# Kernel tuning notes

Measured on AMD Instinct MI355X. Metric: run time of the kernel, lower is better.

## Reference

```python
import jax, jax.numpy as jnp
import numpy as np
import math

B, N, D, H = 4, 512, 256, 8
DH = D // H


def setup_inputs() -> dict:
    key = jax.random.key(0)
    ks = jax.random.split(key, 10)
    s = 1.0 / math.sqrt(D)
    return {
        "h": jax.random.normal(ks[0], (B, N, D), jnp.float32),
        "p": jax.random.uniform(ks[1], (B, N, 2), jnp.float32) * 100.0,
        "side_id": jax.random.randint(ks[2], (B, N), 0, 2),
        "mask": jnp.ones((B, N), dtype=bool),
        # weights stored in 'apply' orientation: y = x @ W (+ b)
        "Wq": jax.random.normal(ks[3], (D, D), jnp.float32) * s,
        "Wk": jax.random.normal(ks[4], (D, D), jnp.float32) * s,
        "Wv": jax.random.normal(ks[5], (D, D), jnp.float32) * s,
        "Wo": jax.random.normal(ks[6], (D, D), jnp.float32) * s,
        "W1": jax.random.normal(ks[7], (4, D), jnp.float32) * 0.5,
        "b1": jnp.zeros((D,), jnp.float32),
        "W2": jax.random.normal(ks[8], (D, H), jnp.float32) * s,
        "b2": jnp.zeros((H,), jnp.float32),
    }


def reference(h, p, side_id, mask, Wq, Wk, Wv, Wo, W1, b1, W2, b2):
    # zero out masked players
    h = jnp.where(mask[..., None], h, 0.0)  # [B,N,D]

    q = (h @ Wq).reshape(B, N, H, DH)
    k = (h @ Wk).reshape(B, N, H, DH)
    v = (h @ Wv).reshape(B, N, H, DH)

    # pairwise relative-position features [B,N,N,4]
    dp = p[:, :, None, :] - p[:, None, :, :]               # [B,N,N,2]
    dist = jnp.clip(jnp.linalg.norm(dp, axis=-1, keepdims=True), 1e-6)
    is_team = (side_id[:, :, None] == side_id[:, None, :]).astype(h.dtype)[..., None]
    feat = jnp.concatenate([dp, dist, is_team], axis=-1)

    # 2-layer bias MLP -> per-head bias [B,H,N,N]
    hid = jax.nn.relu(feat @ W1 + b1)                      # [B,N,N,D]
    bias = (hid @ W2 + b2).transpose(0, 3, 1, 2)           # [B,H,N,N]

    logits = jnp.einsum('bihd,bjhd->bhij', q, k) / math.sqrt(DH)
    logits = logits + bias
    logits = logits + jnp.where(mask, 0.0, -1e9)[:, None, None, :]  # key mask

    attn = jax.nn.softmax(logits, axis=-1)                 # dropout = identity (eval)
    out = jnp.einsum('bhij,bjhd->bihd', attn, v).reshape(B, N, D)
    return out @ Wo
```

## Files before the change

kernel.cpp:

```cpp
#include <hip/hip_runtime.h>
#include <math.h>

#define BB 4
#define NN 512
#define DD 256
#define HH 8
#define BND (BB*NN*DD)

typedef _Float16 h2 __attribute__((ext_vector_type(2)));
typedef _Float16 f16x4 __attribute__((ext_vector_type(4)));
typedef float    f32x4 __attribute__((ext_vector_type(4)));

static __device__ __forceinline__ h2 u2h(unsigned u) { return __builtin_bit_cast(h2, u); }
static __device__ __forceinline__ h2 pk2(float a, float b) {
    h2 r; r[0] = (_Float16)a; r[1] = (_Float16)b; return r;
}
static __device__ __forceinline__ unsigned pk2u(float a, float b) {
    return __builtin_bit_cast(unsigned, pk2(a, b));
}
static __device__ __forceinline__ h2 pkz(float a, float b) {
    return __builtin_bit_cast(h2, __builtin_amdgcn_cvt_pkrtz(a, b));
}
static __device__ __forceinline__ float dot2(h2 a, h2 b, float c) {
    return __builtin_amdgcn_fdot2(a, b, c, false);
}

constexpr int RB = 4;

__global__ __launch_bounds__(256) void qkv_proj(
    const float* __restrict__ hg, const int* __restrict__ mask,
    const float* __restrict__ Wq, const float* __restrict__ Wk, const float* __restrict__ Wv,
    _Float16* __restrict__ q16, _Float16* __restrict__ k16, _Float16* __restrict__ v16h)
{
    __shared__ float hsT[DD][RB];
    const int t = threadIdx.x;
    const int r0 = blockIdx.x * RB;
    #pragma unroll
    for (int rr = 0; rr < RB; ++rr) {
        float x = hg[(size_t)(r0 + rr) * DD + t];
        if (mask[r0 + rr] == 0) x = 0.f;
        hsT[t][rr] = x;
    }
    __syncthreads();
    float aq[RB], ak[RB], av[RB];
    #pragma unroll
    for (int rr = 0; rr < RB; ++rr) { aq[rr] = 0.f; ak[rr] = 0.f; av[rr] = 0.f; }
    for (int d = 0; d < DD; ++d) {
        const float wq = Wq[d*DD + t];
        const float wk = Wk[d*DD + t];
        const float wv = Wv[d*DD + t];
        const float4 h0 = *(const float4*)&hsT[d][0];
        const float hv[4] = {h0.x, h0.y, h0.z, h0.w};
        #pragma unroll
        for (int rr = 0; rr < RB; ++rr) {
            aq[rr] = fmaf(hv[rr], wq, aq[rr]);
            ak[rr] = fmaf(hv[rr], wk, ak[rr]);
            av[rr] = fmaf(hv[rr], wv, av[rr]);
        }
    }
    const float qscale = 0.17677669529663687f;
    #pragma unroll
    for (int rr = 0; rr < RB; ++rr) {
        const int r = r0 + rr;
        q16[(size_t)r*DD + t] = (_Float16)aq[rr];
        k16[(size_t)r*DD + t] = (_Float16)(ak[rr] * qscale);
        v16h[((size_t)(r >> 1)*DD + t)*2 + (r & 1)] = (_Float16)av[rr];
    }
}

__global__ __launch_bounds__(256, 2) void bias_qk(
    const _Float16* __restrict__ q16, const _Float16* __restrict__ k16,
    const float* __restrict__ p, const int* __restrict__ side, const int* __restrict__ mask,
    const float* __restrict__ W1, const float* __restrict__ b1,
    const float* __restrict__ W2, const float* __restrict__ b2,
    unsigned* __restrict__ logitsH)
{
    __shared__ float bsm[4][16*132];
    __shared__ float pis[16][2];
    __shared__ int   sis[16];

    const int t  = threadIdx.x;
    const int w  = t >> 6;
    const int l  = t & 63;
    const int lo = l & 15;
    const int g  = l >> 4;

    const int bid = blockIdx.x;
    const int b   = bid >> 7;
    const int it  = (bid >> 2) & 31;
    const int jq  = bid & 3;
    const int i0  = it * 16;
    const int j0  = jq * 128;

    if (t < 16) {
        const float2 pp = ((const float2*)p)[b*NN + i0 + t];
        pis[t][0] = pp.x; pis[t][1] = pp.y;
        sis[t] = side[b*NN + i0 + t];
    }
    __syncthreads();

    const f16x4 z4 = {(_Float16)0.f,(_Float16)0.f,(_Float16)0.f,(_Float16)0.f};
    const f32x4 zf = {0.f,0.f,0.f,0.f};
    const h2 zz = {(_Float16)0.f, (_Float16)0.f};

    f16x4 a1[16];
    #pragma unroll
    for (int m = 0; m < 16; ++m) {
        const int hid = m*16 + lo;
        f16x4 v = z4;
        const float w0 = W1[hid], w1 = W1[256+hid], w2 = W1[512+hid], w3 = W1[768+hid];
        const float bb1 = b1[hid];
        if (g == 0) { v[0]=(_Float16)w0; v[1]=(_Float16)w1; v[2]=(_Float16)w2; v[3]=(_Float16)w3; }
        else if (g == 1) { v[0]=(_Float16)bb1; }
        a1[m] = v;
    }
    f16x4 a2[16];
    #pragma unroll
    for (int s = 0; s < 16; ++s) {
        const int kb4 = s*16 + g*4;
        const int hs  = lo & 7;
        f16x4 v;
        v[0] = (_Float16)W2[(kb4+0)*HH + hs];
        v[1] = (_Float16)W2[(kb4+1)*HH + hs];
        v[2] = (_Float16)W2[(kb4+2)*HH + hs];
        v[3] = (_Float16)W2[(kb4+3)*HH + hs];
        a2[s] = (lo < 8) ? v : z4;
    }
    float b2v[4];
    #pragma unroll
    for (int r = 0; r < 4; ++r) b2v[r] = (g < 2) ? b2[(g*4 + r) & 7] : 0.f;

    const _Float16* qbase = q16 + (size_t)(b*NN + i0 + lo)*DD;
    f16x4 qf[8][2];
    #pragma unroll
    for (int h = 0; h < 8; ++h) {
        qf[h][0] = *(const f16x4*)(qbase + h*32 + g*4);
        qf[h][1] = *(const f16x4*)(qbase + h*32 + 16 + g*4);
    }

    float* bw = &bsm[w][0];

    for (int jt = w; jt < 8; jt += 4) {
        const int jb = j0 + jt*16;
        const int j  = jb + lo;

        const _Float16* kbase = k16 + (size_t)(b*NN + j)*DD;
        const float2 pj = ((const float2*)p)[b*NN + j];
        const int   sj  = side[b*NN + j];
        const float km  = mask[b*NN + j] ? 0.f : -3.0e4f;

        f32x4 qk[8];
        #pragma unroll
        for (int h = 0; h < 8; ++h) {
            const f16x4 kf0 = *(const f16x4*)(kbase + h*32 + g*4);
            const f16x4 kf1 = *(const f16x4*)(kbase + h*32 + 16 + g*4);
            f32x4 a = __builtin_amdgcn_mfma_f32_16x16x16f16(qf[h][0], kf0, zf, 0, 0, 0);
            qk[h]   = __builtin_amdgcn_mfma_f32_16x16x16f16(qf[h][1], kf1, a, 0, 0, 0);
        }

        #pragma unroll 4
        for (int i = 0; i < 16; ++i) {
            const float pix = pis[i][0], piy = pis[i][1];
            const int   sii = sis[i];
            const float dx = pix - pj.x;
            const float dy = piy - pj.y;
            const float di = fmaxf(sqrtf(dx*dx + dy*dy), 1e-6f);
            const float tm = (sii == sj) ? 1.f : 0.f;
            const h2 fA = pk2(dx, dy);
            const h2 fB = pk2(di, tm);
            f16x4 bf = z4;
            if (g == 0) { bf[0]=fA[0]; bf[1]=fA[1]; bf[2]=fB[0]; bf[3]=fB[1]; }
            else if (g == 1) { bf[0] = (_Float16)1.f; }

            f32x4 e0 = zf, e1 = zf;
            #pragma unroll
            for (int s = 0; s < 16; ++s) {
                const f32x4 c1 = __builtin_amdgcn_mfma_f32_16x16x16f16(a1[s], bf, zf, 0, 0, 0);
                const h2 p01 = pkz(c1[0], c1[1]);
                const h2 p23 = pkz(c1[2], c1[3]);
                const h2 r01 = __builtin_elementwise_max(p01, zz);
                const h2 r23 = __builtin_elementwise_max(p23, zz);
                f16x4 hb;
                hb[0]=r01[0]; hb[1]=r01[1]; hb[2]=r23[0]; hb[3]=r23[1];
                if (s & 1) e1 = __builtin_amdgcn_mfma_f32_16x16x16f16(a2[s], hb, e1, 0, 0, 0);
                else       e0 = __builtin_amdgcn_mfma_f32_16x16x16f16(a2[s], hb, e0, 0, 0, 0);
            }
            if (l < 32) {
                #pragma unroll
                for (int r = 0; r < 4; ++r)
                    bw[i*132 + (g*4 + r)*16 + lo] = e0[r] + e1[r] + b2v[r] + km;
            }
        }

        asm volatile("s_waitcnt lgkmcnt(0)" ::: "memory");
        __builtin_amdgcn_sched_barrier(0);

        #pragma unroll
        for (int h = 0; h < 8; ++h) {
            #pragma unroll
            for (int r = 0; r < 4; ++r)
                bw[(g*4 + r)*132 + h*16 + lo] += qk[h][r];
        }

        asm volatile("s_waitcnt lgkmcnt(0)" ::: "memory");
        __builtin_amdgcn_sched_barrier(0);

        {
            const int hh = (l >> 3) & 7;
            const int jp = l & 7;
            #pragma unroll
            for (int u = 0; u < 16; ++u) {
                const float2 v2 = *(const float2*)&bw[u*132 + hh*16 + 2*jp];
                logitsH[((size_t)((b*NN + i0 + u)*HH + hh))*(NN/2) + (jb >> 1) + jp] =
                    pk2u(v2.x, v2.y);
            }
        }
        asm volatile("s_waitcnt lgkmcnt(0)" ::: "memory");
        __builtin_amdgcn_sched_barrier(0);
    }
}

__global__ __launch_bounds__(256, 4) void attn_sm(
    const unsigned* __restrict__ logitsH, const unsigned* __restrict__ v16p,
    float* __restrict__ ao)
{
    __shared__ unsigned Lgh[16][260];
    __shared__ float red[16][16];
    __shared__ float mx[16];
    __shared__ float rs[16];

    const int t  = threadIdx.x;
    const int b  = blockIdx.x / (NN/2);
    const int i0 = (blockIdx.x % (NN/2)) * 2;

    #pragma unroll
    for (int ii = 0; ii < 2; ++ii)
        #pragma unroll
        for (int hh = 0; hh < HH; ++hh)
            Lgh[ii*8 + hh][t] = logitsH[((size_t)((b*NN + i0 + ii)*HH + hh))*(NN/2) + t];
    __syncthreads();

    const int combo = t >> 4;
    const int sub   = t & 15;
    {
        h2 pm = u2h(0xFC00FC00u);
        for (int jp = sub; jp < NN/2; jp += 16)
            pm = __builtin_elementwise_max(pm, u2h(Lgh[combo][jp]));
        red[combo][sub] = fmaxf((float)pm[0], (float)pm[1]);
    }
    __syncthreads();
    if (t < 16) {
        float mm = red[t][0];
        #pragma unroll
        for (int s = 1; s < 16; ++s) mm = fmaxf(mm, red[t][s]);
        mx[t] = mm;
    }
    __syncthreads();
    {
        const float M = mx[combo];
        float s = 0.f;
        for (int jp = sub; jp < NN/2; jp += 16) {
            const h2 lg = u2h(Lgh[combo][jp]);
            const float e0 = __expf((float)lg[0] - M);
            const float e1 = __expf((float)lg[1] - M);
            s += e0 + e1;
            Lgh[combo][jp] = pk2u(e0, e1);
        }
        red[combo][sub] = s;
    }
    __syncthreads();
    if (t < 16) {
        float s = 0.f;
        #pragma unroll
        for (int ss = 0; ss < 16; ++ss) s += red[t][ss];
        rs[t] = 1.f / s;
    }
    __syncthreads();

    {
        const int c = t;
        const int hh = c >> 5;
        const unsigned* vb = v16p + (size_t)b*(NN/2)*DD + c;
        float o[2] = {0.f, 0.f};
        for (int jp = 0; jp < NN/2; ++jp) {
            const h2 vp = u2h(vb[(size_t)jp*DD]);
            #pragma unroll
            for (int ii = 0; ii < 2; ++ii)
                o[ii] = dot2(u2h(Lgh[ii*8 + hh][jp]), vp, o[ii]);
        }
        #pragma unroll
        for (int ii = 0; ii < 2; ++ii)
            ao[(size_t)(b*NN + i0 + ii)*DD + c] = o[ii] * rs[ii*8 + hh];
    }
}

__global__ __launch_bounds__(256) void oproj(
    const float* __restrict__ X, const float* __restrict__ W, float* __restrict__ Y)
{
    __shared__ float xsT[DD][RB];
    const int t = threadIdx.x;
    const int r0 = blockIdx.x * RB;
    #pragma unroll
    for (int rr = 0; rr < RB; ++rr)
        xsT[t][rr] = X[(size_t)(r0 + rr)*DD + t];
    __syncthreads();
    float a[RB];
    #pragma unroll
    for (int rr = 0; rr < RB; ++rr) a[rr] = 0.f;
    for (int d = 0; d < DD; ++d) {
        const float w = W[d*DD + t];
        const float4 h0 = *(const float4*)&xsT[d][0];
        const float hv[4] = {h0.x, h0.y, h0.z, h0.w};
        #pragma unroll
        for (int rr = 0; rr < RB; ++rr)
            a[rr] = fmaf(hv[rr], w, a[rr]);
    }
    #pragma unroll
    for (int rr = 0; rr < RB; ++rr)
        Y[(size_t)(r0 + rr)*DD + t] = a[rr];
}

extern "C" void kernel_launch(void* const* d_in, const int* in_sizes, int n_in,
                              void* d_out, int out_size, void* d_ws, size_t ws_size,
                              hipStream_t stream) {
    const float* hg   = (const float*)d_in[0];
    const float* p    = (const float*)d_in[1];
    const int*   side = (const int*)d_in[2];
    const int*   mask = (const int*)d_in[3];
    const float* Wq   = (const float*)d_in[4];
    const float* Wk   = (const float*)d_in[5];
    const float* Wv   = (const float*)d_in[6];
    const float* Wo   = (const float*)d_in[7];
    const float* W1   = (const float*)d_in[8];
    const float* b1   = (const float*)d_in[9];
    const float* W2   = (const float*)d_in[10];
    const float* b2   = (const float*)d_in[11];

    float* ws = (float*)d_ws;
    float* ao = ws;
    _Float16* q16 = (_Float16*)(ws + BND);
    _Float16* k16 = q16 + BND;
    _Float16* v16 = k16 + BND;
    unsigned* logitsH = (unsigned*)(v16 + BND);

    qkv_proj<<<(BB*NN)/RB, 256, 0, stream>>>(hg, mask, Wq, Wk, Wv, q16, k16, v16);
    bias_qk<<<512, 256, 0, stream>>>(q16, k16, p, side, mask, W1, b1, W2, b2, logitsH);
    attn_sm<<<BB*(NN/2), 256, 0, stream>>>(logitsH, (const unsigned*)v16, ao);
    oproj<<<(BB*NN)/RB, 256, 0, stream>>>(ao, Wo, (float*)d_out);
}
```

Measured before the change: 101.6 us.

## Use MFMA fp16 GEMMs for QKV and output projections, split bias_qk finer

```diff
diff --git a/kernel.cpp b/kernel.cpp
--- a/kernel.cpp
+++ b/kernel.cpp
@@ -25,50 +25,82 @@
     return __builtin_amdgcn_fdot2(a, b, c, false);
 }
 
-constexpr int RB = 4;
-
-__global__ __launch_bounds__(256) void qkv_proj(
+__global__ __launch_bounds__(256) void pack_wt(
+    const float* __restrict__ Wq, const float* __restrict__ Wk,
+    const float* __restrict__ Wv, const float* __restrict__ Wo,
+    _Float16* __restrict__ wt)
+{
+    __shared__ float T[64][65];
+    const int t  = threadIdx.x;
+    const int nb = blockIdx.x >> 2;
+    const int kb = blockIdx.x & 3;
+    const int tn = t & 63;
+    const int tr = t >> 6;
+    const int nbase = nb * 64;
+    const float* W = (nbase < 256) ? Wq : (nbase < 512) ? Wk : (nbase < 768) ? Wv : Wo;
+    const int noff = nbase & 255;
+    #pragma unroll
+    for (int r = 0; r < 16; ++r) {
+        const int kl = tr*16 + r;
+        T[kl][tn] = W[(size_t)(kb*64 + kl)*DD + noff + tn];
+    }
+    __syncthreads();
+    #pragma unroll
+    for (int r = 0; r < 16; ++r) {
+        const int nl = tr*16 + r;
+        wt[(size_t)(nbase + nl)*DD + kb*64 + tn] = (_Float16)T[tn][nl];
+    }
+}
+
+__global__ __launch_bounds__(64) void gemm_qkv(
     const float* __restrict__ hg, const int* __restrict__ mask,
-    const float* __restrict__ Wq, const float* __restrict__ Wk, const float* __restrict__ Wv,
+    const _Float16* __restrict__ wt,
     _Float16* __restrict__ q16, _Float16* __restrict__ k16, _Float16* __restrict__ v16h)
 {
-    __shared__ float hsT[DD][RB];
-    const int t = threadIdx.x;
-    const int r0 = blockIdx.x * RB;
-    #pragma unroll
-    for (int rr = 0; rr < RB; ++rr) {
-        float x = hg[(size_t)(r0 + rr) * DD + t];
-        if (mask[r0 + rr] == 0) x = 0.f;
-        hsT[t][rr] = x;
-    }
-    __syncthreads();
-    float aq[RB], ak[RB], av[RB];
-    #pragma unroll
-    for (int rr = 0; rr < RB; ++rr) { aq[rr] = 0.f; ak[rr] = 0.f; av[rr] = 0.f; }
-    for (int d = 0; d < DD; ++d) {
-        const float wq = Wq[d*DD + t];
-        const float wk = Wk[d*DD + t];
-        const float wv = Wv[d*DD + t];
-        const float4 h0 = *(const float4*)&hsT[d][0];
-        const float hv[4] = {h0.x, h0.y, h0.z, h0.w};
-        #pragma unroll
-        for (int rr = 0; rr < RB; ++rr) {
-            aq[rr] = fmaf(hv[rr], wq, aq[rr]);
-            ak[rr] = fmaf(hv[rr], wk, ak[rr]);
-            av[rr] = fmaf(hv[rr], wv, av[rr]);
-        }
+    const int l  = threadIdx.x;
+    const int lo = l & 15, g = l >> 4;
+    const int bid = blockIdx.x;
+    const int rt = bid / 24, ct = bid % 24;
+    const int R0 = rt*16, C0 = ct*32;
+    const int row = R0 + lo;
+    const float msc = (mask[row] != 0) ? 1.f : 0.f;
+
+    const float*    xrow = hg + (size_t)row*DD;
+    const _Float16* w0   = wt + (size_t)(C0 + lo)*DD;
+    const _Float16* w1   = wt + (size_t)(C0 + 16 + lo)*DD;
+    f32x4 ac0 = {0.f,0.f,0.f,0.f}, ac1 = {0.f,0.f,0.f,0.f};
+    #pragma unroll
+    for (int kk = 0; kk < 16; ++kk) {
+        const float4 xv = *(const float4*)(xrow + kk*16 + g*4);
+        f16x4 a;
+        a[0] = (_Float16)(xv.x * msc);
+        a[1] = (_Float16)(xv.y * msc);
+        a[2] = (_Float16)(xv.z * msc);
+        a[3] = (_Float16)(xv.w * msc);
+        const f16x4 b0 = *(const f16x4*)(w0 + kk*16 + g*4);
+        const f16x4 b1 = *(const f16x4*)(w1 + kk*16 + g*4);
+        ac0 = __builtin_amdgcn_mfma_f32_16x16x16f16(a, b0, ac0, 0, 0, 0);
+        ac1 = __builtin_amdgcn_mfma_f32_16x16x16f16(a, b1, ac1, 0, 0, 0);
     }
     const float qscale = 0.17677669529663687f;
     #pragma unroll
-    for (int rr = 0; rr < RB; ++rr) {
-        const int r = r0 + rr;
-        q16[(size_t)r*DD + t] = (_Float16)aq[rr];
-        k16[(size_t)r*DD + t] = (_Float16)(ak[rr] * qscale);
-        v16h[((size_t)(r >> 1)*DD + t)*2 + (r & 1)] = (_Float16)av[rr];
-    }
-}
-
-__global__ __launch_bounds__(256, 2) void bias_qk(
+    for (int ci = 0; ci < 2; ++ci) {
+        const f32x4 ac = ci ? ac1 : ac0;
+        const int col = C0 + ci*16 + lo;
+        const int seg = col >> 8;
+        const int cc  = col & 255;
+        #pragma unroll
+        for (int r = 0; r < 4; ++r) {
+            const int ro = R0 + g*4 + r;
+            const float val = ac[r];
+            if (seg == 0)      q16[(size_t)ro*DD + cc] = (_Float16)val;
+            else if (seg == 1) k16[(size_t)ro*DD + cc] = (_Float16)(val * qscale);
+            else               v16h[((size_t)(ro >> 1)*DD + cc)*2 + (ro & 1)] = (_Float16)val;
+        }
+    }
+}
+
+__global__ __launch_bounds__(256, 4) void bias_qk(
     const _Float16* __restrict__ q16, const _Float16* __restrict__ k16,
     const float* __restrict__ p, const int* __restrict__ side, const int* __restrict__ mask,
     const float* __restrict__ W1, const float* __restrict__ b1,
@@ -86,11 +118,11 @@
     const int g  = l >> 4;
 
     const int bid = blockIdx.x;
-    const int b   = bid >> 7;
-    const int it  = (bid >> 2) & 31;
-    const int jq  = bid & 3;
+    const int b   = bid >> 8;
+    const int it  = (bid >> 3) & 31;
+    const int je  = bid & 7;
     const int i0  = it * 16;
-    const int j0  = jq * 128;
+    const int j0  = je * 64;
 
     if (t < 16) {
         const float2 pp = ((const float2*)p)[b*NN + i0 + t];
@@ -140,7 +172,7 @@
 
     float* bw = &bsm[w][0];
 
-    for (int jt = w; jt < 8; jt += 4) {
+    for (int jt = w; jt < 4; jt += 4) {
         const int jb = j0 + jt*16;
         const int j  = jb + lo;
 
@@ -294,30 +326,42 @@
     }
 }
 
-__global__ __launch_bounds__(256) void oproj(
-    const float* __restrict__ X, const float* __restrict__ W, float* __restrict__ Y)
-{
-    __shared__ float xsT[DD][RB];
-    const int t = threadIdx.x;
-    const int r0 = blockIdx.x * RB;
-    #pragma unroll
-    for (int rr = 0; rr < RB; ++rr)
-        xsT[t][rr] = X[(size_t)(r0 + rr)*DD + t];
-    __syncthreads();
-    float a[RB];
-    #pragma unroll
-    for (int rr = 0; rr < RB; ++rr) a[rr] = 0.f;
-    for (int d = 0; d < DD; ++d) {
-        const float w = W[d*DD + t];
-        const float4 h0 = *(const float4*)&xsT[d][0];
-        const float hv[4] = {h0.x, h0.y, h0.z, h0.w};
-        #pragma unroll
-        for (int rr = 0; rr < RB; ++rr)
-            a[rr] = fmaf(hv[rr], w, a[rr]);
-    }
-    #pragma unroll
-    for (int rr = 0; rr < RB; ++rr)
-        Y[(size_t)(r0 + rr)*DD + t] = a[rr];
+__global__ __launch_bounds__(64) void gemm_o(
+    const float* __restrict__ X, const _Float16* __restrict__ wt,
+    float* __restrict__ Y)
+{
+    const int l  = threadIdx.x;
+    const int lo = l & 15, g = l >> 4;
+    const int bid = blockIdx.x;
+    const int rt = bid >> 3, ct = bid & 7;
+    const int R0 = rt*16, C0 = ct*32;
+    const int row = R0 + lo;
+
+    const float*    xrow = X + (size_t)row*DD;
+    const _Float16* w0   = wt + (size_t)(C0 + lo)*DD;
+    const _Float16* w1   = wt + (size_t)(C0 + 16 + lo)*DD;
+    f32x4 ac0 = {0.f,0.f,0.f,0.f}, ac1 = {0.f,0.f,0.f,0.f};
+    #pragma unroll
+    for (int kk = 0; kk < 16; ++kk) {
+        const float4 xv = *(const float4*)(xrow + kk*16 + g*4);
+        f16x4 a;
+        a[0] = (_Float16)xv.x;
+        a[1] = (_Float16)xv.y;
+        a[2] = (_Float16)xv.z;
+        a[3] = (_Float16)xv.w;
+        const f16x4 b0 = *(const f16x4*)(w0 + kk*16 + g*4);
+        const f16x4 b1 = *(const f16x4*)(w1 + kk*16 + g*4);
+        ac0 = __builtin_amdgcn_mfma_f32_16x16x16f16(a, b0, ac0, 0, 0, 0);
+        ac1 = __builtin_amdgcn_mfma_f32_16x16x16f16(a, b1, ac1, 0, 0, 0);
+    }
+    #pragma unroll
+    for (int ci = 0; ci < 2; ++ci) {
+        const f32x4 ac = ci ? ac1 : ac0;
+        const int col = C0 + ci*16 + lo;
+        #pragma unroll
+        for (int r = 0; r < 4; ++r)
+            Y[(size_t)(R0 + g*4 + r)*DD + col] = ac[r];
+    }
 }
 
 extern "C" void kernel_launch(void* const* d_in, const int* in_sizes, int n_in,
@@ -342,9 +386,11 @@
     _Float16* k16 = q16 + BND;
     _Float16* v16 = k16 + BND;
     unsigned* logitsH = (unsigned*)(v16 + BND);
-
-    qkv_proj<<<(BB*NN)/RB, 256, 0, stream>>>(hg, mask, Wq, Wk, Wv, q16, k16, v16);
-    bias_qk<<<512, 256, 0, stream>>>(q16, k16, p, side, mask, W1, b1, W2, b2, logitsH);
+    _Float16* wt16 = (_Float16*)(logitsH + (size_t)BB*NN*HH*(NN/2));
+
+    pack_wt<<<64, 256, 0, stream>>>(Wq, Wk, Wv, Wo, wt16);
+    gemm_qkv<<<128*24, 64, 0, stream>>>(hg, mask, wt16, q16, k16, v16);
+    bias_qk<<<1024, 256, 0, stream>>>(q16, k16, p, side, mask, W1, b1, W2, b2, logitsH);
     attn_sm<<<BB*(NN/2), 256, 0, stream>>>(logitsH, (const unsigned*)v16, ao);
-    oproj<<<(BB*NN)/RB, 256, 0, stream>>>(ao, Wo, (float*)d_out);
-}
+    gemm_o<<<128*8, 64, 0, stream>>>(ao, wt16 + (size_t)768*DD, (float*)d_out);
+}
```

After: 99.17 us. 1.02x faster.
